# Kernel tuning notes

Measured on AMD Instinct MI355X. Metric: run time of the kernel, lower is better.

The kernel has to match this reference:

```python
import jax, jax.numpy as jnp
import numpy as np

NUM_GRAPHS = 256
BN_EPS = 1e-5


def _bn(x, gamma, beta):
    # torch BatchNorm1d training-mode forward: biased batch stats
    m = jnp.mean(x, axis=0)
    v = jnp.mean((x - m) ** 2, axis=0)
    return (x - m) * jax.lax.rsqrt(v + BN_EPS) * gamma + beta


def setup_inputs() -> dict:
    key = jax.random.key(0)
    ks = jax.random.split(key, 12)
    N, D, S = 400000, 128, 64
    h = jax.random.normal(ks[0], (N, D), dtype=jnp.float32)
    sub = jax.random.normal(ks[1], (N, S), dtype=jnp.float32)
    batch = jnp.sort(jax.random.randint(ks[2], (N,), 0, NUM_GRAPHS, dtype=jnp.int32))
    sc = lambda fan_in: 1.0 / np.sqrt(fan_in)
    return {
        "h": h, "sub": sub, "batch": batch,
        # sub_enhance: Linear(S, D) + BN(D) + ReLU
        "W1": jax.random.uniform(ks[3], (S, D), jnp.float32, -sc(S), sc(S)),
        "b1": jnp.zeros((D,), jnp.float32),
        "g1": jnp.ones((D,), jnp.float32),
        "be1": jnp.zeros((D,), jnp.float32),
        # gate: Linear(2D, D) + Sigmoid
        "Wg": jax.random.uniform(ks[4], (2 * D, D), jnp.float32, -sc(2 * D), sc(2 * D)),
        "bg": jnp.zeros((D,), jnp.float32),
        # score_mlp: Linear(2D, D) + BN + ReLU + Linear(D, 1)
        "Ws1": jax.random.uniform(ks[5], (2 * D, D), jnp.float32, -sc(2 * D), sc(2 * D)),
        "bs1": jnp.zeros((D,), jnp.float32),
        "g2": jnp.ones((D,), jnp.float32),
        "be2": jnp.zeros((D,), jnp.float32),
        "Ws2": jax.random.uniform(ks[6], (D, 1), jnp.float32, -sc(D), sc(D)),
        "bs2": jnp.zeros((1,), jnp.float32),
        "mix": jnp.float32(0.5),
    }


def reference(h, sub, batch, W1, b1, g1, be1, Wg, bg, Ws1, bs1, g2, be2, Ws2, bs2, mix):
    G = NUM_GRAPHS
    # counts per graph, guard against empty segments
    counts = jax.ops.segment_sum(jnp.ones_like(batch, jnp.float32), batch, num_segments=G)
    counts = jnp.maximum(counts, 1.0)[:, None]  # [G,1]

    sub_enhanced = jax.nn.relu(_bn(sub @ W1 + b1, g1, be1))  # [N,D]
    gate_weight = jax.nn.sigmoid(jnp.concatenate([h, sub_enhanced], axis=1) @ Wg + bg)
    h_fused = h + gate_weight * sub_enhanced  # [N,D]

    graph_mean = jax.ops.segment_sum(h, batch, num_segments=G) / counts  # [G,D]
    h_sq_mean = jax.ops.segment_sum(h * h, batch, num_segments=G) / counts
    graph_std = jnp.sqrt(jnp.maximum(h_sq_mean - graph_mean ** 2, 1e-8))
    h_dev = (h - graph_mean[batch]) / (graph_std[batch] + 1e-8)  # [N,D]

    z = jax.nn.relu(_bn(jnp.concatenate([h_fused, h_dev], axis=1) @ Ws1 + bs1, g2, be2))
    score_logit = z @ Ws2 + bs2  # [N,1]

    # scatter_softmax over batch segments
    seg_max = jax.ops.segment_max(score_logit, batch, num_segments=G)  # [G,1]
    e = jnp.exp(score_logit - seg_max[batch])
    denom = jax.ops.segment_sum(e, batch, num_segments=G)[batch]
    score = e / denom  # [N,1]

    weighted_fused = jax.ops.segment_sum(h_fused * score, batch, num_segments=G)  # [G,D]
    weighted_orig = graph_mean
    alpha = jax.nn.sigmoid(mix)
    return alpha * weighted_fused + (1.0 - alpha) * weighted_orig
```

## Files before the change

### kernel.cpp

```cpp
#include <hip/hip_runtime.h>

#define DD 128
#define SS 64
#define GG 256
#define LTDA 264
#define LTDS 72

typedef short short8 __attribute__((ext_vector_type(8)));
typedef float f32x4 __attribute__((ext_vector_type(4)));

__device__ __forceinline__ unsigned short f2bf(float x) {
  unsigned u = __float_as_uint(x);
  u += 0x7FFFu + ((u >> 16) & 1u);
  return (unsigned short)(u >> 16);
}
__device__ __forceinline__ float bf2f(unsigned short b) {
  return __uint_as_float(((unsigned)b) << 16);
}
__device__ __forceinline__ unsigned pkbf(float lo, float hi) {
  unsigned r;
  asm("v_cvt_pk_bf16_f32 %0, %1, %2" : "=v"(r) : "v"(lo), "v"(hi));
  return r;
}
__device__ __forceinline__ float fsig(float x) {
  return __builtin_amdgcn_rcpf(1.f + __expf(-x));
}

__device__ __forceinline__ void stage8k(const unsigned short* __restrict__ g,
                                        unsigned short* l, int tid) {
  int wave = tid >> 6;
  const unsigned* gp = (const unsigned*)g;
  unsigned* lp = (unsigned*)l;
  __builtin_amdgcn_global_load_lds(
      (const __attribute__((address_space(1))) unsigned*)(gp + tid * 4),
      (__attribute__((address_space(3))) unsigned*)(lp + wave * 256), 16, 0, 0);
  __builtin_amdgcn_global_load_lds(
      (const __attribute__((address_space(1))) unsigned*)(gp + 1024 + tid * 4),
      (__attribute__((address_space(3))) unsigned*)(lp + 1024 + wave * 256), 16, 0, 0);
}

__device__ __forceinline__ void mfma8(const unsigned short* __restrict__ Abase,
                                      int astride,
                                      const unsigned short* __restrict__ wst,
                                      int k0, int m16, int quad, int mts,
                                      int nts, f32x4 acc[2][4]) {
  short8 af[2];
  af[0] = *(const short8*)(Abase + (size_t)((mts + 0) * 16 + m16) * astride + k0 + quad * 8);
  af[1] = *(const short8*)(Abase + (size_t)((mts + 1) * 16 + m16) * astride + k0 + quad * 8);
  short8 bf[4];
#pragma unroll
  for (int ni = 0; ni < 4; ++ni) {
    int n = (nts + ni) * 16 + m16;
    int s = (quad + (n >> 1)) & 3;
    bf[ni] = *(const short8*)(wst + n * 32 + s * 8);
  }
#pragma unroll
  for (int mi = 0; mi < 2; ++mi)
#pragma unroll
    for (int ni = 0; ni < 4; ++ni)
      acc[mi][ni] = __builtin_amdgcn_mfma_f32_16x16x32_bf16(af[mi], bf[ni],
                                                            acc[mi][ni], 0, 0, 0);
}

__device__ __forceinline__ void mfma8t(const unsigned short* __restrict__ wst,
                                       const unsigned short* __restrict__ Abase,
                                       int k0, int m16, int quad, int mts,
                                       int nts, f32x4 acc[4][2]) {
  short8 wfr[4];
#pragma unroll
  for (int mi = 0; mi < 4; ++mi) {
    int ch = (mts + mi) * 16 + m16;
    int s = (quad + (ch >> 1)) & 3;
    wfr[mi] = *(const short8*)(wst + ch * 32 + s * 8);
  }
  short8 xf[2];
#pragma unroll
  for (int ni = 0; ni < 2; ++ni) {
    int row = (nts + ni) * 16 + m16;
    xf[ni] = *(const short8*)(Abase + (size_t)row * LTDA + k0 + quad * 8);
  }
#pragma unroll
  for (int mi = 0; mi < 4; ++mi)
#pragma unroll
    for (int ni = 0; ni < 2; ++ni)
      acc[mi][ni] = __builtin_amdgcn_mfma_f32_16x16x32_bf16(wfr[mi], xf[ni],
                                                            acc[mi][ni], 0, 0, 0);
}

__global__ void w_prep(const float* __restrict__ W1, const float* __restrict__ Wg,
                       const float* __restrict__ Ws1, unsigned short* __restrict__ w1t,
                       unsigned short* __restrict__ wgt, unsigned short* __restrict__ ws1t) {
  int cb = blockIdx.x;
  const float* W;
  unsigned short* out;
  int kb;
  if (cb < 2) { W = W1; out = w1t; kb = cb; }
  else if (cb < 10) { W = Wg; out = wgt; kb = cb - 2; }
  else { W = Ws1; out = ws1t; kb = cb - 10; }
  out += (size_t)kb * 4096;
  int i = threadIdx.x;
#pragma unroll
  for (int t = 0; t < 2; ++t) {
    int u = i * 2 + t;
    int n = u >> 2, s = u & 3;
    int kc = (s - (n >> 1)) & 3;
    int kbase = kb * 32 + kc * 8;
    unsigned short* o = out + u * 8;
#pragma unroll
    for (int j = 0; j < 8; ++j) o[j] = f2bf(W[(size_t)(kbase + j) * DD + n]);
  }
}

__global__ __launch_bounds__(256, 4) void k1_fused(
    const float* __restrict__ sub, const unsigned short* __restrict__ w1t,
    const float* __restrict__ b1, float* __restrict__ bn1s,
    float* __restrict__ bn1q, const float* __restrict__ h,
    const int* __restrict__ batch, float* __restrict__ gsum,
    float* __restrict__ gsq, float* __restrict__ counts, int N, int nB1) {
  __shared__ unsigned short subbuf[64][LTDS];
  __shared__ unsigned short wstage[2][4096];
  __shared__ float bn1l[256];
  int tid = threadIdx.x;

  if (blockIdx.x >= nB1) {
    int* bc = (int*)bn1l;
    int row0 = (blockIdx.x - nB1) * 256;
    {
      int row = row0 + tid;
      bc[tid] = (row < N) ? batch[row] : -1;
    }
    __syncthreads();
    int stripe = tid >> 5, c4 = (tid & 31) * 4;
    float sx = 0, sy = 0, sz = 0, sw = 0, qx = 0, qy = 0, qz = 0, qw = 0, cnt = 0;
    int gcur = -1;
    int lrow = stripe;
    bool valid = bc[lrow] >= 0;
    float4 v;
    if (valid) v = *(const float4*)&h[(size_t)(row0 + lrow) * DD + c4];
    for (int it = 0; it < 32; ++it) {
      if (!valid) break;
      int g = bc[lrow];
      int nrow = lrow + 8;
      bool nvalid = (it < 31) && (bc[nrow] >= 0);
      float4 vn;
      if (nvalid) vn = *(const float4*)&h[(size_t)(row0 + nrow) * DD + c4];
      if (g != gcur) {
        if (gcur >= 0) {
          float* gp = &gsum[(size_t)gcur * DD + c4];
          float* qp = &gsq[(size_t)gcur * DD + c4];
          atomicAdd(gp + 0, sx); atomicAdd(gp + 1, sy);
          atomicAdd(gp + 2, sz); atomicAdd(gp + 3, sw);
          atomicAdd(qp + 0, qx); atomicAdd(qp + 1, qy);
          atomicAdd(qp + 2, qz); atomicAdd(qp + 3, qw);
          if ((tid & 31) == 0) atomicAdd(&counts[gcur], cnt);
        }
        gcur = g;
        sx = sy = sz = sw = qx = qy = qz = qw = cnt = 0.f;
      }
      sx += v.x; sy += v.y; sz += v.z; sw += v.w;
      qx = fmaf(v.x, v.x, qx); qy = fmaf(v.y, v.y, qy);
      qz = fmaf(v.z, v.z, qz); qw = fmaf(v.w, v.w, qw);
      cnt += 1.f;
      v = vn; lrow = nrow; valid = nvalid;
    }
    if (gcur >= 0) {
      float* gp = &gsum[(size_t)gcur * DD + c4];
      float* qp = &gsq[(size_t)gcur * DD + c4];
      atomicAdd(gp + 0, sx); atomicAdd(gp + 1, sy);
      atomicAdd(gp + 2, sz); atomicAdd(gp + 3, sw);
      atomicAdd(qp + 0, qx); atomicAdd(qp + 1, qy);
      atomicAdd(qp + 2, qz); atomicAdd(qp + 3, qw);
      if ((tid & 31) == 0) atomicAdd(&counts[gcur], cnt);
    }
    return;
  }

  int row0 = blockIdx.x * 64;
  bn1l[tid] = 0.f;
  for (int i = tid; i < 1024; i += 256) {
    int r = i >> 4, c = (i & 15) * 4;
    float4 v = *(const float4*)&sub[(size_t)(row0 + r) * SS + c];
    uint2 uu;
    uu.x = pkbf(v.x, v.y);
    uu.y = pkbf(v.z, v.w);
    *(uint2*)&subbuf[r][c] = uu;
  }
  stage8k(w1t, &wstage[0][0], tid);
  stage8k(w1t + 4096, &wstage[1][0], tid);
  __syncthreads();
  int lane = tid & 63, wave = tid >> 6;
  int m16 = lane & 15, quad = lane >> 4;
  int mts = 2 * (wave & 1), nts = 4 * (wave >> 1);
  f32x4 acc[2][4];
#pragma unroll
  for (int mi = 0; mi < 2; ++mi)
#pragma unroll
    for (int ni = 0; ni < 4; ++ni) acc[mi][ni] = (f32x4){0.f, 0.f, 0.f, 0.f};
  mfma8(&subbuf[0][0], LTDS, &wstage[0][0], 0, m16, quad, mts, nts, acc);
  mfma8(&subbuf[0][0], LTDS, &wstage[1][0], 32, m16, quad, mts, nts, acc);
#pragma unroll
  for (int ni = 0; ni < 4; ++ni) {
    int col = (nts + ni) * 16 + m16;
    float b1c = b1[col];
    float s = 0.f, q = 0.f;
#pragma unroll
    for (int mi = 0; mi < 2; ++mi)
#pragma unroll
      for (int r = 0; r < 4; ++r) {
        float x = acc[mi][ni][r] + b1c;
        s += x;
        q += x * x;
      }
    s += __shfl_down(s, 32); s += __shfl_down(s, 16);
    q += __shfl_down(q, 32); q += __shfl_down(q, 16);
    if (lane < 16) {
      atomicAdd(&bn1l[col], s);
      atomicAdd(&bn1l[128 + col], q);
    }
  }
  __syncthreads();
  if (tid < 128) {
    atomicAdd(&bn1s[tid], bn1l[tid]);
    atomicAdd(&bn1q[tid], bn1l[128 + tid]);
  }
}

__global__ void k2a_bn_final(const float* __restrict__ s, const float* __restrict__ q,
                             const float* __restrict__ gamma, const float* __restrict__ beta,
                             float* __restrict__ sc, float* __restrict__ sh, float Nf) {
  int d = threadIdx.x;
  float m = s[d] / Nf;
  float v = q[d] / Nf - m * m;
  float r = rsqrtf(v + 1e-5f);
  float scv = gamma[d] * r;
  sc[d] = scv;
  sh[d] = beta[d] - m * scv;
}

__global__ void k2_fused(const float* __restrict__ bn1s, const float* __restrict__ bn1q,
                         const float* __restrict__ g1, const float* __restrict__ be1,
                         float* __restrict__ sc1, float* __restrict__ sh1, float Nf,
                         const float* __restrict__ gsum, const float* __restrict__ gsq,
                         const float* __restrict__ counts, float* __restrict__ gmean,
                         float* __restrict__ grstd) {
  int d = threadIdx.x;
  if (blockIdx.x == 0) {
    float m = bn1s[d] / Nf;
    float v = bn1q[d] / Nf - m * m;
    float r = rsqrtf(v + 1e-5f);
    float scv = g1[d] * r;
    sc1[d] = scv;
    sh1[d] = be1[d] - m * scv;
  } else {
    int g = blockIdx.x - 1;
    float c = counts[g];
    float cf = c > 1.f ? c : 1.f;
    size_t idx = (size_t)g * DD + d;
    float m = gsum[idx] / cf;
    float v = gsq[idx] / cf - m * m;
    float sd = sqrtf(fmaxf(v, 1e-8f));
    gmean[idx] = m;
    grstd[idx] = 1.f / (sd + 1e-8f);
  }
}

__global__ __launch_bounds__(256, 3) void k3_main(
    const float* __restrict__ h, const float* __restrict__ sub,
    const int* __restrict__ batch, const unsigned short* __restrict__ w1t,
    const unsigned short* __restrict__ wgt, const unsigned short* __restrict__ ws1t,
    const float* __restrict__ b1, const float* __restrict__ sc1,
    const float* __restrict__ sh1, const float* __restrict__ bg,
    const float* __restrict__ bs1, const float* __restrict__ gmean,
    const float* __restrict__ grstd, float* __restrict__ hfused,
    unsigned short* __restrict__ zp16, float* __restrict__ bn2s,
    float* __restrict__ bn2q, int N) {
  __shared__ unsigned short abuf[64][LTDA];
  __shared__ unsigned short wstage[2][4096];
  __shared__ int bt[64];
  int tid = threadIdx.x;
  int row0 = blockIdx.x * 64;

#pragma unroll
  for (int t = 0; t < 4; ++t) {
    int u = tid + t * 256;
    int r = u >> 4, c8 = (u & 15) * 8;
    const float* hp = &h[(size_t)(row0 + r) * DD + c8];
    float4 v0 = *(const float4*)hp, v1 = *(const float4*)(hp + 4);
    uint4 uu;
    uu.x = pkbf(v0.x, v0.y);
    uu.y = pkbf(v0.z, v0.w);
    uu.z = pkbf(v1.x, v1.y);
    uu.w = pkbf(v1.z, v1.w);
    *(uint4*)&abuf[r][c8] = uu;
  }
#pragma unroll
  for (int t = 0; t < 2; ++t) {
    int u = tid + t * 256;
    int r = u >> 3, c8 = (u & 7) * 8;
    const float* sp = &sub[(size_t)(row0 + r) * SS + c8];
    float4 v0 = *(const float4*)sp, v1 = *(const float4*)(sp + 4);
    uint4 uu;
    uu.x = pkbf(v0.x, v0.y);
    uu.y = pkbf(v0.z, v0.w);
    uu.z = pkbf(v1.x, v1.y);
    uu.w = pkbf(v1.z, v1.w);
    *(uint4*)&abuf[r][128 + c8] = uu;
  }
  if (tid < 64) bt[tid] = batch[row0 + tid];
  stage8k(w1t, &wstage[0][0], tid);
  stage8k(w1t + 4096, &wstage[1][0], tid);
  __syncthreads();

  int lane = tid & 63, wave = tid >> 6;
  int m16 = lane & 15, quad = lane >> 4;
  int mts = 4 * (wave >> 1), nts = 2 * (wave & 1);
  f32x4 acc[4][2];

#pragma unroll
  for (int mi = 0; mi < 4; ++mi)
#pragma unroll
    for (int ni = 0; ni < 2; ++ni) acc[mi][ni] = (f32x4){0.f, 0.f, 0.f, 0.f};
  mfma8t(&wstage[0][0], &abuf[0][0], 128, m16, quad, mts, nts, acc);
  mfma8t(&wstage[1][0], &abuf[0][0], 160, m16, quad, mts, nts, acc);
  __syncthreads();
  stage8k(wgt, &wstage[0][0], tid);
#pragma unroll
  for (int mi = 0; mi < 4; ++mi) {
    int ch0 = (mts + mi) * 16 + quad * 4;
    float4 b1v = *(const float4*)&b1[ch0];
    float4 s1v = *(const float4*)&sc1[ch0];
    float4 h1v = *(const float4*)&sh1[ch0];
#pragma unroll
    for (int ni = 0; ni < 2; ++ni) {
      int row = (nts + ni) * 16 + m16;
      float se0 = fmaxf(fmaf(acc[mi][ni][0] + b1v.x, s1v.x, h1v.x), 0.f);
      float se1 = fmaxf(fmaf(acc[mi][ni][1] + b1v.y, s1v.y, h1v.y), 0.f);
      float se2 = fmaxf(fmaf(acc[mi][ni][2] + b1v.z, s1v.z, h1v.z), 0.f);
      float se3 = fmaxf(fmaf(acc[mi][ni][3] + b1v.w, s1v.w, h1v.w), 0.f);
      uint2 uu;
      uu.x = pkbf(se0, se1);
      uu.y = pkbf(se2, se3);
      *(uint2*)&abuf[row][128 + ch0] = uu;
    }
  }
  __syncthreads();

#pragma unroll
  for (int mi = 0; mi < 4; ++mi)
#pragma unroll
    for (int ni = 0; ni < 2; ++ni) acc[mi][ni] = (f32x4){0.f, 0.f, 0.f, 0.f};
#pragma unroll 1
  for (int c = 0; c < 8; ++c) {
    if (c < 7) stage8k(wgt + (size_t)(c + 1) * 4096, &wstage[(c + 1) & 1][0], tid);
    mfma8t(&wstage[c & 1][0], &abuf[0][0], c * 32, m16, quad, mts, nts, acc);
    __syncthreads();
  }
  stage8k(ws1t, &wstage[0][0], tid);
#pragma unroll
  for (int mi = 0; mi < 4; ++mi) {
    int ch0 = (mts + mi) * 16 + quad * 4;
    float4 bgv = *(const float4*)&bg[ch0];
#pragma unroll
    for (int ni = 0; ni < 2; ++ni) {
      int row = (nts + ni) * 16 + m16;
      int grow = row0 + row;
      float4 hv = *(const float4*)&h[(size_t)grow * DD + ch0];
      uint2 seu = *(const uint2*)&abuf[row][128 + ch0];
      int g = bt[row];
      float4 gm = *(const float4*)&gmean[(size_t)g * DD + ch0];
      float4 gr = *(const float4*)&grstd[(size_t)g * DD + ch0];
      float g0 = fsig(acc[mi][ni][0] + bgv.x);
      float g1v = fsig(acc[mi][ni][1] + bgv.y);
      float g2 = fsig(acc[mi][ni][2] + bgv.z);
      float g3 = fsig(acc[mi][ni][3] + bgv.w);
      float hf0 = fmaf(g0, bf2f((unsigned short)(seu.x & 0xffff)), hv.x);
      float hf1 = fmaf(g1v, bf2f((unsigned short)(seu.x >> 16)), hv.y);
      float hf2 = fmaf(g2, bf2f((unsigned short)(seu.y & 0xffff)), hv.z);
      float hf3 = fmaf(g3, bf2f((unsigned short)(seu.y >> 16)), hv.w);
      float hd0 = (hv.x - gm.x) * gr.x;
      float hd1 = (hv.y - gm.y) * gr.y;
      float hd2 = (hv.z - gm.z) * gr.z;
      float hd3 = (hv.w - gm.w) * gr.w;
      float4 hfv = {hf0, hf1, hf2, hf3};
      *(float4*)&hfused[(size_t)grow * DD + ch0] = hfv;
      uint2 uf, ud;
      uf.x = pkbf(hf0, hf1);
      uf.y = pkbf(hf2, hf3);
      ud.x = pkbf(hd0, hd1);
      ud.y = pkbf(hd2, hd3);
      *(uint2*)&abuf[row][ch0] = uf;
      *(uint2*)&abuf[row][128 + ch0] = ud;
    }
  }
  __syncthreads();

#pragma unroll
  for (int mi = 0; mi < 4; ++mi)
#pragma unroll
    for (int ni = 0; ni < 2; ++ni) acc[mi][ni] = (f32x4){0.f, 0.f, 0.f, 0.f};
#pragma unroll 1
  for (int c = 0; c < 8; ++c) {
    if (c < 7) stage8k(ws1t + (size_t)(c + 1) * 4096, &wstage[(c + 1) & 1][0], tid);
    mfma8t(&wstage[c & 1][0], &abuf[0][0], c * 32, m16, quad, mts, nts, acc);
    __syncthreads();
  }
  float* scr = (float*)&abuf[0][0];
  int srow = (wave & 1) * 16 + m16;
#pragma unroll
  for (int mi = 0; mi < 4; ++mi) {
    int ch0 = (mts + mi) * 16 + quad * 4;
    float4 bsv = *(const float4*)&bs1[ch0];
    f32x4 s4 = (f32x4){0.f, 0.f, 0.f, 0.f};
    f32x4 q4 = (f32x4){0.f, 0.f, 0.f, 0.f};
#pragma unroll
    for (int ni = 0; ni < 2; ++ni) {
      int grow = row0 + (nts + ni) * 16 + m16;
      float z0 = acc[mi][ni][0] + bsv.x;
      float z1 = acc[mi][ni][1] + bsv.y;
      float z2 = acc[mi][ni][2] + bsv.z;
      float z3 = acc[mi][ni][3] + bsv.w;
      uint2 uz;
      uz.x = pkbf(z0, z1);
      uz.y = pkbf(z2, z3);
      *(uint2*)&zp16[(size_t)grow * DD + ch0] = uz;
      s4[0] += z0; s4[1] += z1; s4[2] += z2; s4[3] += z3;
      q4[0] = fmaf(z0, z0, q4[0]); q4[1] = fmaf(z1, z1, q4[1]);
      q4[2] = fmaf(z2, z2, q4[2]); q4[3] = fmaf(z3, z3, q4[3]);
    }
    *(f32x4*)&scr[srow * 132 + ch0] = s4;
    *(f32x4*)&scr[4224 + srow * 132 + ch0] = q4;
  }
  __syncthreads();
  if (tid < 128) {
    float s = 0.f, q = 0.f;
#pragma unroll 4
    for (int i = 0; i < 32; ++i) {
      s += scr[i * 132 + tid];
      q += scr[4224 + i * 132 + tid];
    }
    atomicAdd(&bn2s[tid], s);
    atomicAdd(&bn2q[tid], q);
  }
}

__global__ __launch_bounds__(256, 8) void k56_score(
    const unsigned short* __restrict__ zp16, const float* __restrict__ hf,
    const int* __restrict__ batch, const float* __restrict__ sc2,
    const float* __restrict__ sh2, const float* __restrict__ Ws2,
    const float* __restrict__ bs2, float* __restrict__ denom,
    float* __restrict__ wf, int N) {
  __shared__ int bc[256];
  int tid = threadIdx.x;
  int row0 = blockIdx.x * 256;
  {
    int row = row0 + tid;
    bc[tid] = (row < N) ? batch[row] : -1;
  }
  __syncthreads();
  int stripe = tid >> 5, c4 = (tid & 31) * 4;
  float4 s2 = *(const float4*)&sc2[c4];
  float4 h2 = *(const float4*)&sh2[c4];
  float4 w2 = *(const float4*)&Ws2[c4];
  float b2 = bs2[0];
  float ax = 0, ay = 0, az = 0, aw = 0, ds = 0;
  int gcur = -1;
  int lrow = stripe;
  bool valid = bc[lrow] >= 0;
  uint2 vz;
  float4 vh;
  if (valid) {
    vz = *(const uint2*)&zp16[(size_t)(row0 + lrow) * DD + c4];
    vh = *(const float4*)&hf[(size_t)(row0 + lrow) * DD + c4];
  }
  for (int it = 0; it < 32; ++it) {
    if (!valid) break;
    int g = bc[lrow];
    int nrow = lrow + 8;
    bool nvalid = (it < 31) && (bc[nrow] >= 0);
    uint2 vzn;
    float4 vhn;
    if (nvalid) {
      vzn = *(const uint2*)&zp16[(size_t)(row0 + nrow) * DD + c4];
      vhn = *(const float4*)&hf[(size_t)(row0 + nrow) * DD + c4];
    }
    if (g != gcur) {
      if (gcur >= 0) {
        float* wp = &wf[(size_t)gcur * DD + c4];
        atomicAdd(wp + 0, ax); atomicAdd(wp + 1, ay);
        atomicAdd(wp + 2, az); atomicAdd(wp + 3, aw);
        if ((tid & 31) == 0) atomicAdd(&denom[gcur], ds);
      }
      gcur = g;
      ax = ay = az = aw = ds = 0.f;
    }
    float z0 = bf2f((unsigned short)(vz.x & 0xffff));
    float z1 = bf2f((unsigned short)(vz.x >> 16));
    float z2 = bf2f((unsigned short)(vz.y & 0xffff));
    float z3 = bf2f((unsigned short)(vz.y >> 16));
    float p = fmaxf(fmaf(z0, s2.x, h2.x), 0.f) * w2.x;
    p = fmaf(fmaxf(fmaf(z1, s2.y, h2.y), 0.f), w2.y, p);
    p = fmaf(fmaxf(fmaf(z2, s2.z, h2.z), 0.f), w2.z, p);
    p = fmaf(fmaxf(fmaf(z3, s2.w, h2.w), 0.f), w2.w, p);
    p += __shfl_xor(p, 16); p += __shfl_xor(p, 8);
    p += __shfl_xor(p, 4);  p += __shfl_xor(p, 2);
    p += __shfl_xor(p, 1);
    float e = __expf(p + b2);
    ax = fmaf(vh.x, e, ax); ay = fmaf(vh.y, e, ay);
    az = fmaf(vh.z, e, az); aw = fmaf(vh.w, e, aw);
    ds += e;
    vz = vzn; vh = vhn; lrow = nrow; valid = nvalid;
  }
  if (gcur >= 0) {
    float* wp = &wf[(size_t)gcur * DD + c4];
    atomicAdd(wp + 0, ax); atomicAdd(wp + 1, ay);
    atomicAdd(wp + 2, az); atomicAdd(wp + 3, aw);
    if ((tid & 31) == 0) atomicAdd(&denom[gcur], ds);
  }
}

__global__ void k7_out(const float* __restrict__ wf, const float* __restrict__ denom,
                       const float* __restrict__ gmean, const float* __restrict__ mix,
                       float* __restrict__ out) {
  int g = blockIdx.x, d = threadIdx.x;
  float alpha = 1.f / (1.f + expf(-mix[0]));
  float dn = denom[g];
  size_t idx = (size_t)g * DD + d;
  float w = (dn > 0.f) ? wf[idx] / dn : 0.f;
  out[idx] = alpha * w + (1.f - alpha) * gmean[idx];
}

extern "C" void kernel_launch(void* const* d_in, const int* in_sizes, int n_in,
                              void* d_out, int out_size, void* d_ws, size_t ws_size,
                              hipStream_t stream) {
  const float* h   = (const float*)d_in[0];
  const float* sub = (const float*)d_in[1];
  const int* batch = (const int*)d_in[2];
  const float* W1  = (const float*)d_in[3];
  const float* b1  = (const float*)d_in[4];
  const float* g1  = (const float*)d_in[5];
  const float* be1 = (const float*)d_in[6];
  const float* Wg  = (const float*)d_in[7];
  const float* bg  = (const float*)d_in[8];
  const float* Ws1 = (const float*)d_in[9];
  const float* bs1 = (const float*)d_in[10];
  const float* g2  = (const float*)d_in[11];
  const float* be2 = (const float*)d_in[12];
  const float* Ws2 = (const float*)d_in[13];
  const float* bs2 = (const float*)d_in[14];
  const float* mix = (const float*)d_in[15];
  float* out = (float*)d_out;
  const int N = in_sizes[0] / DD;
  const int nB1 = N / 64;
  const int nBG = (N + 255) / 256;

  float* ws = (float*)d_ws;
  size_t off = 0;
  float* hf    = ws + off; off += (size_t)N * DD;
  unsigned short* zp16 = (unsigned short*)(ws + off); off += (size_t)N * DD / 2;
  float* zbase = ws + off;
  float* gsum  = ws + off; off += (size_t)GG * DD;
  float* gsq   = ws + off; off += (size_t)GG * DD;
  float* wf    = ws + off; off += (size_t)GG * DD;
  float* bn1s  = ws + off; off += 128;
  float* bn1q  = ws + off; off += 128;
  float* bn2s  = ws + off; off += 128;
  float* bn2q  = ws + off; off += 128;
  float* counts = ws + off; off += GG;
  float* denom  = ws + off; off += GG;
  size_t zcount = (size_t)(ws + off - zbase);
  float* gmean = ws + off; off += (size_t)GG * DD;
  float* grstd = ws + off; off += (size_t)GG * DD;
  float* sc1 = ws + off; off += 128;
  float* sh1 = ws + off; off += 128;
  float* sc2 = ws + off; off += 128;
  float* sh2 = ws + off; off += 128;
  unsigned short* w1t  = (unsigned short*)(ws + off); off += 8192 / 2;
  unsigned short* wgt  = (unsigned short*)(ws + off); off += 32768 / 2;
  unsigned short* ws1t = (unsigned short*)(ws + off); off += 32768 / 2;

  hipMemsetAsync(zbase, 0, zcount * sizeof(float), stream);
  w_prep<<<18, 256, 0, stream>>>(W1, Wg, Ws1, w1t, wgt, ws1t);

  k1_fused<<<nB1 + nBG, 256, 0, stream>>>(sub, w1t, b1, bn1s, bn1q,
                                          h, batch, gsum, gsq, counts, N, nB1);
  k2_fused<<<1 + GG, 128, 0, stream>>>(bn1s, bn1q, g1, be1, sc1, sh1, (float)N,
                                       gsum, gsq, counts, gmean, grstd);

  k3_main<<<nB1, 256, 0, stream>>>(h, sub, batch, w1t, wgt, ws1t, b1, sc1, sh1,
                                   bg, bs1, gmean, grstd, hf, zp16, bn2s, bn2q, N);

  k2a_bn_final<<<1, 128, 0, stream>>>(bn2s, bn2q, g2, be2, sc2, sh2, (float)N);
  k56_score<<<nBG, 256, 0, stream>>>(zp16, hf, batch, sc2, sh2, Ws2, bs2,
                                     denom, wf, N);
  k7_out<<<GG, 128, 0, stream>>>(wf, denom, gmean, mix, out);
}
```

Measured before the change: 846.4 us.

## Split fused k1 into separate kernels and deepen row prefetch in streaming passes

Splits the combined GEMM-stats/segment-stats kernel k1_fused into two kernels, k1_bn and k1_graph, so each can have its own occupancy bound (6 and 8 waves per SIMD). Both the graph-statistics pass and the score/softmax pass now keep four rows of loads in flight per thread instead of one, to hide global memory latency. k56_score's occupancy bound is lowered from 8 to 6 to make room for the extra prefetch registers. The split adds a kernel launch, gives up running the two kinds of blocks concurrently within one grid, and raises register pressure.

```diff
diff --git a/kernel.cpp b/kernel.cpp
--- a/kernel.cpp
+++ b/kernel.cpp
@@ -111,70 +111,14 @@
   }
 }
 
-__global__ __launch_bounds__(256, 4) void k1_fused(
+__global__ __launch_bounds__(256, 6) void k1_bn(
     const float* __restrict__ sub, const unsigned short* __restrict__ w1t,
     const float* __restrict__ b1, float* __restrict__ bn1s,
-    float* __restrict__ bn1q, const float* __restrict__ h,
-    const int* __restrict__ batch, float* __restrict__ gsum,
-    float* __restrict__ gsq, float* __restrict__ counts, int N, int nB1) {
+    float* __restrict__ bn1q) {
   __shared__ unsigned short subbuf[64][LTDS];
   __shared__ unsigned short wstage[2][4096];
   __shared__ float bn1l[256];
   int tid = threadIdx.x;
-
-  if (blockIdx.x >= nB1) {
-    int* bc = (int*)bn1l;
-    int row0 = (blockIdx.x - nB1) * 256;
-    {
-      int row = row0 + tid;
-      bc[tid] = (row < N) ? batch[row] : -1;
-    }
-    __syncthreads();
-    int stripe = tid >> 5, c4 = (tid & 31) * 4;
-    float sx = 0, sy = 0, sz = 0, sw = 0, qx = 0, qy = 0, qz = 0, qw = 0, cnt = 0;
-    int gcur = -1;
-    int lrow = stripe;
-    bool valid = bc[lrow] >= 0;
-    float4 v;
-    if (valid) v = *(const float4*)&h[(size_t)(row0 + lrow) * DD + c4];
-    for (int it = 0; it < 32; ++it) {
-      if (!valid) break;
-      int g = bc[lrow];
-      int nrow = lrow + 8;
-      bool nvalid = (it < 31) && (bc[nrow] >= 0);
-      float4 vn;
-      if (nvalid) vn = *(const float4*)&h[(size_t)(row0 + nrow) * DD + c4];
-      if (g != gcur) {
-        if (gcur >= 0) {
-          float* gp = &gsum[(size_t)gcur * DD + c4];
-          float* qp = &gsq[(size_t)gcur * DD + c4];
-          atomicAdd(gp + 0, sx); atomicAdd(gp + 1, sy);
-          atomicAdd(gp + 2, sz); atomicAdd(gp + 3, sw);
-          atomicAdd(qp + 0, qx); atomicAdd(qp + 1, qy);
-          atomicAdd(qp + 2, qz); atomicAdd(qp + 3, qw);
-          if ((tid & 31) == 0) atomicAdd(&counts[gcur], cnt);
-        }
-        gcur = g;
-        sx = sy = sz = sw = qx = qy = qz = qw = cnt = 0.f;
-      }
-      sx += v.x; sy += v.y; sz += v.z; sw += v.w;
-      qx = fmaf(v.x, v.x, qx); qy = fmaf(v.y, v.y, qy);
-      qz = fmaf(v.z, v.z, qz); qw = fmaf(v.w, v.w, qw);
-      cnt += 1.f;
-      v = vn; lrow = nrow; valid = nvalid;
-    }
-    if (gcur >= 0) {
-      float* gp = &gsum[(size_t)gcur * DD + c4];
-      float* qp = &gsq[(size_t)gcur * DD + c4];
-      atomicAdd(gp + 0, sx); atomicAdd(gp + 1, sy);
-      atomicAdd(gp + 2, sz); atomicAdd(gp + 3, sw);
-      atomicAdd(qp + 0, qx); atomicAdd(qp + 1, qy);
-      atomicAdd(qp + 2, qz); atomicAdd(qp + 3, qw);
-      if ((tid & 31) == 0) atomicAdd(&counts[gcur], cnt);
-    }
-    return;
-  }
-
   int row0 = blockIdx.x * 64;
   bn1l[tid] = 0.f;
   for (int i = tid; i < 1024; i += 256) {
@@ -222,6 +166,73 @@
   if (tid < 128) {
     atomicAdd(&bn1s[tid], bn1l[tid]);
     atomicAdd(&bn1q[tid], bn1l[128 + tid]);
+  }
+}
+
+__global__ __launch_bounds__(256, 8) void k1_graph(
+    const float* __restrict__ h, const int* __restrict__ batch,
+    float* __restrict__ gsum, float* __restrict__ gsq,
+    float* __restrict__ counts, int N) {
+  __shared__ int bc[256];
+  int tid = threadIdx.x;
+  int row0 = blockIdx.x * 256;
+  {
+    int row = row0 + tid;
+    bc[tid] = (row < N) ? batch[row] : -1;
+  }
+  __syncthreads();
+  int stripe = tid >> 5, c4 = (tid & 31) * 4;
+  float sx = 0, sy = 0, sz = 0, sw = 0, qx = 0, qy = 0, qz = 0, qw = 0, cnt = 0;
+  int gcur = -1;
+  float4 vbuf[4];
+  bool vval[4];
+#pragma unroll
+  for (int j = 0; j < 4; ++j) {
+    int r = stripe + 8 * j;
+    vval[j] = bc[r] >= 0;
+    if (vval[j]) vbuf[j] = *(const float4*)&h[(size_t)(row0 + r) * DD + c4];
+  }
+#pragma unroll 1
+  for (int mit = 0; mit < 8; ++mit) {
+#pragma unroll
+    for (int j = 0; j < 4; ++j) {
+      int it = mit * 4 + j;
+      int r = stripe + 8 * it;
+      bool valid = vval[j];
+      float4 v = vbuf[j];
+      bool nv = (it + 4 < 32) && (bc[r + 32] >= 0);
+      vval[j] = nv;
+      if (nv) vbuf[j] = *(const float4*)&h[(size_t)(row0 + r + 32) * DD + c4];
+      if (valid) {
+        int g = bc[r];
+        if (g != gcur) {
+          if (gcur >= 0) {
+            float* gp = &gsum[(size_t)gcur * DD + c4];
+            float* qp = &gsq[(size_t)gcur * DD + c4];
+            atomicAdd(gp + 0, sx); atomicAdd(gp + 1, sy);
+            atomicAdd(gp + 2, sz); atomicAdd(gp + 3, sw);
+            atomicAdd(qp + 0, qx); atomicAdd(qp + 1, qy);
+            atomicAdd(qp + 2, qz); atomicAdd(qp + 3, qw);
+            if ((tid & 31) == 0) atomicAdd(&counts[gcur], cnt);
+          }
+          gcur = g;
+          sx = sy = sz = sw = qx = qy = qz = qw = cnt = 0.f;
+        }
+        sx += v.x; sy += v.y; sz += v.z; sw += v.w;
+        qx = fmaf(v.x, v.x, qx); qy = fmaf(v.y, v.y, qy);
+        qz = fmaf(v.z, v.z, qz); qw = fmaf(v.w, v.w, qw);
+        cnt += 1.f;
+      }
+    }
+  }
+  if (gcur >= 0) {
+    float* gp = &gsum[(size_t)gcur * DD + c4];
+    float* qp = &gsq[(size_t)gcur * DD + c4];
+    atomicAdd(gp + 0, sx); atomicAdd(gp + 1, sy);
+    atomicAdd(gp + 2, sz); atomicAdd(gp + 3, sw);
+    atomicAdd(qp + 0, qx); atomicAdd(qp + 1, qy);
+    atomicAdd(qp + 2, qz); atomicAdd(qp + 3, qw);
+    if ((tid & 31) == 0) atomicAdd(&counts[gcur], cnt);
   }
 }
 
@@ -443,7 +454,7 @@
   }
 }
 
-__global__ __launch_bounds__(256, 8) void k56_score(
+__global__ __launch_bounds__(256, 6) void k56_score(
     const unsigned short* __restrict__ zp16, const float* __restrict__ hf,
     const int* __restrict__ batch, const float* __restrict__ sc2,
     const float* __restrict__ sh2, const float* __restrict__ Ws2,
@@ -464,51 +475,62 @@
   float b2 = bs2[0];
   float ax = 0, ay = 0, az = 0, aw = 0, ds = 0;
   int gcur = -1;
-  int lrow = stripe;
-  bool valid = bc[lrow] >= 0;
-  uint2 vz;
-  float4 vh;
-  if (valid) {
-    vz = *(const uint2*)&zp16[(size_t)(row0 + lrow) * DD + c4];
-    vh = *(const float4*)&hf[(size_t)(row0 + lrow) * DD + c4];
-  }
-  for (int it = 0; it < 32; ++it) {
-    if (!valid) break;
-    int g = bc[lrow];
-    int nrow = lrow + 8;
-    bool nvalid = (it < 31) && (bc[nrow] >= 0);
-    uint2 vzn;
-    float4 vhn;
-    if (nvalid) {
-      vzn = *(const uint2*)&zp16[(size_t)(row0 + nrow) * DD + c4];
-      vhn = *(const float4*)&hf[(size_t)(row0 + nrow) * DD + c4];
-    }
-    if (g != gcur) {
-      if (gcur >= 0) {
-        float* wp = &wf[(size_t)gcur * DD + c4];
-        atomicAdd(wp + 0, ax); atomicAdd(wp + 1, ay);
-        atomicAdd(wp + 2, az); atomicAdd(wp + 3, aw);
-        if ((tid & 31) == 0) atomicAdd(&denom[gcur], ds);
+  uint2 vz[4];
+  float4 vh[4];
+  bool vval[4];
+#pragma unroll
+  for (int j = 0; j < 4; ++j) {
+    int r = stripe + 8 * j;
+    vval[j] = bc[r] >= 0;
+    if (vval[j]) {
+      vz[j] = *(const uint2*)&zp16[(size_t)(row0 + r) * DD + c4];
+      vh[j] = *(const float4*)&hf[(size_t)(row0 + r) * DD + c4];
+    }
+  }
+#pragma unroll 1
+  for (int mit = 0; mit < 8; ++mit) {
+#pragma unroll
+    for (int j = 0; j < 4; ++j) {
+      int it = mit * 4 + j;
+      int r = stripe + 8 * it;
+      bool valid = vval[j];
+      uint2 z2v = vz[j];
+      float4 hv = vh[j];
+      bool nv = (it + 4 < 32) && (bc[r + 32] >= 0);
+      vval[j] = nv;
+      if (nv) {
+        vz[j] = *(const uint2*)&zp16[(size_t)(row0 + r + 32) * DD + c4];
+        vh[j] = *(const float4*)&hf[(size_t)(row0 + r + 32) * DD + c4];
       }
-      gcur = g;
-      ax = ay = az = aw = ds = 0.f;
-    }
-    float z0 = bf2f((unsigned short)(vz.x & 0xffff));
-    float z1 = bf2f((unsigned short)(vz.x >> 16));
-    float z2 = bf2f((unsigned short)(vz.y & 0xffff));
-    float z3 = bf2f((unsigned short)(vz.y >> 16));
-    float p = fmaxf(fmaf(z0, s2.x, h2.x), 0.f) * w2.x;
-    p = fmaf(fmaxf(fmaf(z1, s2.y, h2.y), 0.f), w2.y, p);
-    p = fmaf(fmaxf(fmaf(z2, s2.z, h2.z), 0.f), w2.z, p);
-    p = fmaf(fmaxf(fmaf(z3, s2.w, h2.w), 0.f), w2.w, p);
-    p += __shfl_xor(p, 16); p += __shfl_xor(p, 8);
-    p += __shfl_xor(p, 4);  p += __shfl_xor(p, 2);
-    p += __shfl_xor(p, 1);
-    float e = __expf(p + b2);
-    ax = fmaf(vh.x, e, ax); ay = fmaf(vh.y, e, ay);
-    az = fmaf(vh.z, e, az); aw = fmaf(vh.w, e, aw);
-    ds += e;
-    vz = vzn; vh = vhn; lrow = nrow; valid = nvalid;
+      if (valid) {
+        int g = bc[r];
+        if (g != gcur) {
+          if (gcur >= 0) {
+            float* wp = &wf[(size_t)gcur * DD + c4];
+            atomicAdd(wp + 0, ax); atomicAdd(wp + 1, ay);
+            atomicAdd(wp + 2, az); atomicAdd(wp + 3, aw);
+            if ((tid & 31) == 0) atomicAdd(&denom[gcur], ds);
+          }
+          gcur = g;
+          ax = ay = az = aw = ds = 0.f;
+        }
+        float z0 = bf2f((unsigned short)(z2v.x & 0xffff));
+        float z1 = bf2f((unsigned short)(z2v.x >> 16));
+        float zz2 = bf2f((unsigned short)(z2v.y & 0xffff));
+        float z3 = bf2f((unsigned short)(z2v.y >> 16));
+        float p = fmaxf(fmaf(z0, s2.x, h2.x), 0.f) * w2.x;
+        p = fmaf(fmaxf(fmaf(z1, s2.y, h2.y), 0.f), w2.y, p);
+        p = fmaf(fmaxf(fmaf(zz2, s2.z, h2.z), 0.f), w2.z, p);
+        p = fmaf(fmaxf(fmaf(z3, s2.w, h2.w), 0.f), w2.w, p);
+        p += __shfl_xor(p, 16); p += __shfl_xor(p, 8);
+        p += __shfl_xor(p, 4);  p += __shfl_xor(p, 2);
+        p += __shfl_xor(p, 1);
+        float e = __expf(p + b2);
+        ax = fmaf(hv.x, e, ax); ay = fmaf(hv.y, e, ay);
+        az = fmaf(hv.z, e, az); aw = fmaf(hv.w, e, aw);
+        ds += e;
+      }
+    }
   }
   if (gcur >= 0) {
     float* wp = &wf[(size_t)gcur * DD + c4];
@@ -581,8 +603,8 @@
   hipMemsetAsync(zbase, 0, zcount * sizeof(float), stream);
   w_prep<<<18, 256, 0, stream>>>(W1, Wg, Ws1, w1t, wgt, ws1t);
 
-  k1_fused<<<nB1 + nBG, 256, 0, stream>>>(sub, w1t, b1, bn1s, bn1q,
-                                          h, batch, gsum, gsq, counts, N, nB1);
+  k1_bn<<<nB1, 256, 0, stream>>>(sub, w1t, b1, bn1s, bn1q);
+  k1_graph<<<nBG, 256, 0, stream>>>(h, batch, gsum, gsq, counts, N);
   k2_fused<<<1 + GG, 128, 0, stream>>>(bn1s, bn1q, g1, be1, sc1, sh1, (float)N,
                                        gsum, gsq, counts, gmean, grstd);
 
```

Measured after the change: 898.6 us. 6.2% more time.
